# Kernel tuning notes

Hardware: AMD Instinct MI355X
Metric: run time of the kernel (lower is better)

Reference implementation:

```python
import jax, jax.numpy as jnp
import numpy as np

# The 16 differentiable binary logic gates used by difflogic are all of the form
# c0 + c1*a + c2*b + c3*(a*b). Rows are gate ids 0..15.
GATE_COEF = jnp.array([
    [0., 0., 0., 0.],    # 0: False
    [0., 0., 0., 1.],    # 1: a AND b
    [0., 1., 0., -1.],   # 2: a AND NOT b
    [0., 1., 0., 0.],    # 3: a
    [0., 0., 1., -1.],   # 4: NOT a AND b
    [0., 0., 1., 0.],    # 5: b
    [0., 1., 1., -2.],   # 6: XOR
    [0., 1., 1., -1.],   # 7: OR
    [1., -1., -1., 1.],  # 8: NOR
    [1., -1., -1., 2.],  # 9: XNOR
    [1., 0., -1., 0.],   # 10: NOT b
    [1., 0., -1., 1.],   # 11: a OR NOT b (b implies a)
    [1., -1., 0., 0.],   # 12: NOT a
    [1., -1., 0., 1.],   # 13: NOT a OR b (a implies b)
    [1., 0., 0., -1.],   # 14: NAND
    [1., 0., 0., 0.],    # 15: True
], dtype=jnp.float32)

BATCH = 256
IN_DIM = 1024
WIDTH = 64000
K = 10
TAU = 30.0


def _logic_layer(x, w, idx_a, idx_b):
    # x: [B, in_dim], w: [out, 16], idx_*: [out] int32
    a = x[:, idx_a]            # [B, out]
    b = x[:, idx_b]            # [B, out]
    coef = jax.nn.softmax(w, axis=-1) @ GATE_COEF   # [out, 4]
    return coef[:, 0] + coef[:, 1] * a + coef[:, 2] * b + coef[:, 3] * (a * b)


def setup_inputs() -> dict:
    key = jax.random.key(0)
    ks = jax.random.split(key, 10)
    x = jax.random.uniform(ks[0], (BATCH, IN_DIM), dtype=jnp.float32)
    w1 = jax.random.normal(ks[1], (WIDTH, 16), dtype=jnp.float32)
    w2 = jax.random.normal(ks[2], (WIDTH, 16), dtype=jnp.float32)
    w3 = jax.random.normal(ks[3], (WIDTH, 16), dtype=jnp.float32)
    idx_a1 = jax.random.randint(ks[4], (WIDTH,), 0, IN_DIM, dtype=jnp.int32)
    idx_b1 = jax.random.randint(ks[5], (WIDTH,), 0, IN_DIM, dtype=jnp.int32)
    idx_a2 = jax.random.randint(ks[6], (WIDTH,), 0, WIDTH, dtype=jnp.int32)
    idx_b2 = jax.random.randint(ks[7], (WIDTH,), 0, WIDTH, dtype=jnp.int32)
    idx_a3 = jax.random.randint(ks[8], (WIDTH,), 0, WIDTH, dtype=jnp.int32)
    idx_b3 = jax.random.randint(ks[9], (WIDTH,), 0, WIDTH, dtype=jnp.int32)
    return {"x": x, "w1": w1, "w2": w2, "w3": w3,
            "idx_a1": idx_a1, "idx_b1": idx_b1,
            "idx_a2": idx_a2, "idx_b2": idx_b2,
            "idx_a3": idx_a3, "idx_b3": idx_b3}


def reference(x, w1, w2, w3, idx_a1, idx_b1, idx_a2, idx_b2, idx_a3, idx_b3):
    h = _logic_layer(x, w1, idx_a1, idx_b1)
    h = _logic_layer(h, w2, idx_a2, idx_b2)
    h = _logic_layer(h, w3, idx_a3, idx_b3)
    # GroupSum: [B, WIDTH] -> [B, K, WIDTH//K] -> sum -> / tau
    return h.reshape(h.shape[0], K, -1).sum(axis=-1) / TAU
```

## Files before the change

### kernel.cpp

```cpp
#include <hip/hip_runtime.h>
#include <stdint.h>


#define BATCH   256
#define IN_DIM  1024
#define WIDTH   64000
#define NGROUP  10
#define GSIZE   6400
#define TAU     30.0f
#define NWAVE   8
#define GPW     8
#define GPB     (NWAVE*GPW)
#define NBLK    (WIDTH/GPB)

typedef unsigned short ushort_t;

static __device__ __forceinline__ float bf2f(ushort_t s) {
    return __uint_as_float((uint32_t)s << 16);
}
static __device__ __forceinline__ ushort_t f2bf(float f) {
    uint32_t u = __float_as_uint(f);
    return (ushort_t)((u + 0x7fffu + ((u >> 16) & 1u)) >> 16);
}
static __device__ __forceinline__ float gate1(float4 c, float a, float b) {
    return fmaf(b, fmaf(c.w, a, c.z), fmaf(c.y, a, c.x));
}
static __device__ __forceinline__ float4 gate4(float4 c, float4 a, float4 b) {
    float4 r;
    r.x = gate1(c, a.x, b.x);
    r.y = gate1(c, a.y, b.y);
    r.z = gate1(c, a.z, b.z);
    r.w = gate1(c, a.w, b.w);
    return r;
}
static __device__ __forceinline__ float4 up4(ushort4 s) {
    return make_float4(bf2f(s.x), bf2f(s.y), bf2f(s.z), bf2f(s.w));
}

__global__ __launch_bounds__(256) void transpose_kernel(
    const float* __restrict__ x, ushort_t* __restrict__ xT)
{
    __shared__ float tile[64][65];
    const int c0 = (blockIdx.x & 15) * 64;
    const int b0 = (blockIdx.x >> 4) * 64;
    const int lt = threadIdx.x & 63;
    const int wt = threadIdx.x >> 6;
    for (int r = wt; r < 64; r += 4)
        tile[r][lt] = x[(b0 + r) * IN_DIM + c0 + lt];
    __syncthreads();
    for (int r = wt; r < 64; r += 4)
        xT[(c0 + r) * BATCH + b0 + lt] = f2bf(tile[lt][r]);
}

static __device__ __forceinline__ float4 softmax_coef(const float* __restrict__ w)
{
    const float4* w4 = (const float4*)w;
    float4 q0 = w4[0], q1 = w4[1], q2 = w4[2], q3 = w4[3];
    float p[16] = {q0.x,q0.y,q0.z,q0.w, q1.x,q1.y,q1.z,q1.w,
                   q2.x,q2.y,q2.z,q2.w, q3.x,q3.y,q3.z,q3.w};
    float m = p[0];
    #pragma unroll
    for (int i = 1; i < 16; ++i) m = fmaxf(m, p[i]);
    float s = 0.f;
    #pragma unroll
    for (int i = 0; i < 16; ++i) { p[i] = __expf(p[i] - m); s += p[i]; }
    const float inv = 1.0f / s;
    float c0 = (p[8]+p[9]+p[10]+p[11]+p[12]+p[13]+p[14]+p[15]) * inv;
    float c1 = (p[2]+p[3]+p[6]+p[7] - p[8]-p[9]-p[12]-p[13]) * inv;
    float c2 = (p[4]+p[5]+p[6]+p[7] - p[8]-p[9]-p[10]-p[11]) * inv;
    float c3 = (p[1]-p[2]-p[4]-2.f*p[6]-p[7]+p[8]+2.f*p[9]+p[11]+p[13]-p[14]) * inv;
    return make_float4(c0, c1, c2, c3);
}

__global__ __launch_bounds__(256) void prep_kernel(
    const float* __restrict__ w1, const float* __restrict__ w2,
    const float* __restrict__ w3,
    const int* __restrict__ ia1, const int* __restrict__ ib1,
    const int* __restrict__ ia2, const int* __restrict__ ib2,
    const int* __restrict__ ia3, const int* __restrict__ ib3,
    int* __restrict__ leaf,
    float4* __restrict__ pc)
{
    const int j = blockIdx.x * 256 + threadIdx.x;
    if (j >= WIDTH) return;

    const int pa = ia3[j], pb = ib3[j];
    const int qaa = ia2[pa], qab = ib2[pa];
    const int qba = ia2[pb], qbb = ib2[pb];

    int* L = leaf + (size_t)j * 8;
    L[0] = ia1[qaa]; L[1] = ib1[qaa];
    L[2] = ia1[qab]; L[3] = ib1[qab];
    L[4] = ia1[qba]; L[5] = ib1[qba];
    L[6] = ia1[qbb]; L[7] = ib1[qbb];

    float4* P = pc + (size_t)j * 7;
    P[0] = softmax_coef(w1 + (size_t)qaa * 16);
    P[1] = softmax_coef(w1 + (size_t)qab * 16);
    P[2] = softmax_coef(w1 + (size_t)qba * 16);
    P[3] = softmax_coef(w1 + (size_t)qbb * 16);
    P[4] = softmax_coef(w2 + (size_t)pa * 16);
    P[5] = softmax_coef(w2 + (size_t)pb * 16);
    P[6] = softmax_coef(w3 + (size_t)j * 16);
}

__global__ __launch_bounds__(512, 4) void fused_kernel(
    const ushort_t* __restrict__ xT,
    const int*      __restrict__ leaf,
    const float4*   __restrict__ pc,
    float*          __restrict__ red_out)
{
    __shared__ int    sleaf[GPB * 8];
    __shared__ float4 spc[GPB * 7];
    __shared__ float4 sred[NWAVE][64];

    const int tid = threadIdx.x;

    sleaf[tid] = leaf[(size_t)blockIdx.x * (GPB * 8) + tid];
    if (tid < GPB * 7)
        spc[tid] = pc[(size_t)blockIdx.x * (GPB * 7) + tid];
    __syncthreads();

    const int lane = tid & 63;
    const int wave = tid >> 6;
    const int gbase = wave * GPW;

    float4 acc = make_float4(0.f, 0.f, 0.f, 0.f);

    #pragma unroll 2
    for (int u = 0; u < GPW; ++u) {
        const int g = gbase + u;
        const int l0 = __builtin_amdgcn_readfirstlane(sleaf[g*8 + 0]);
        const int l1 = __builtin_amdgcn_readfirstlane(sleaf[g*8 + 1]);
        const int l2 = __builtin_amdgcn_readfirstlane(sleaf[g*8 + 2]);
        const int l3 = __builtin_amdgcn_readfirstlane(sleaf[g*8 + 3]);
        const int l4 = __builtin_amdgcn_readfirstlane(sleaf[g*8 + 4]);
        const int l5 = __builtin_amdgcn_readfirstlane(sleaf[g*8 + 5]);
        const int l6 = __builtin_amdgcn_readfirstlane(sleaf[g*8 + 6]);
        const int l7 = __builtin_amdgcn_readfirstlane(sleaf[g*8 + 7]);

        const ushort4 v0 = ((const ushort4*)(xT + (size_t)l0 * BATCH))[lane];
        const ushort4 v1 = ((const ushort4*)(xT + (size_t)l1 * BATCH))[lane];
        const ushort4 v2 = ((const ushort4*)(xT + (size_t)l2 * BATCH))[lane];
        const ushort4 v3 = ((const ushort4*)(xT + (size_t)l3 * BATCH))[lane];
        const ushort4 v4 = ((const ushort4*)(xT + (size_t)l4 * BATCH))[lane];
        const ushort4 v5 = ((const ushort4*)(xT + (size_t)l5 * BATCH))[lane];
        const ushort4 v6 = ((const ushort4*)(xT + (size_t)l6 * BATCH))[lane];
        const ushort4 v7 = ((const ushort4*)(xT + (size_t)l7 * BATCH))[lane];

        const float4 C1aa = spc[g*7 + 0];
        const float4 C1ab = spc[g*7 + 1];
        const float4 C1ba = spc[g*7 + 2];
        const float4 C1bb = spc[g*7 + 3];
        const float4 C2a  = spc[g*7 + 4];
        const float4 C2b  = spc[g*7 + 5];
        const float4 C3c  = spc[g*7 + 6];

        const float4 haa = gate4(C1aa, up4(v0), up4(v1));
        const float4 hab = gate4(C1ab, up4(v2), up4(v3));
        const float4 hba = gate4(C1ba, up4(v4), up4(v5));
        const float4 hbb = gate4(C1bb, up4(v6), up4(v7));
        const float4 h2a = gate4(C2a, haa, hab);
        const float4 h2b = gate4(C2b, hba, hbb);
        const float4 h3  = gate4(C3c, h2a, h2b);
        acc.x += h3.x; acc.y += h3.y; acc.z += h3.z; acc.w += h3.w;
    }

    sred[wave][lane] = acc;
    __syncthreads();
    if (wave == 0) {
        float4 t = sred[0][lane];
        #pragma unroll
        for (int w = 1; w < NWAVE; ++w) {
            float4 q = sred[w][lane];
            t.x += q.x; t.y += q.y; t.z += q.z; t.w += q.w;
        }
        const float sc = 1.0f / TAU;
        const int grp = (blockIdx.x * GPB) / GSIZE;
        const int b0 = lane * 4;
        atomicAdd(&red_out[(b0 + 0) * NGROUP + grp], t.x * sc);
        atomicAdd(&red_out[(b0 + 1) * NGROUP + grp], t.y * sc);
        atomicAdd(&red_out[(b0 + 2) * NGROUP + grp], t.z * sc);
        atomicAdd(&red_out[(b0 + 3) * NGROUP + grp], t.w * sc);
    }
}

extern "C" void kernel_launch(void* const* d_in, const int* in_sizes, int n_in,
                              void* d_out, int out_size, void* d_ws, size_t ws_size,
                              hipStream_t stream)
{
    const float* x   = (const float*)d_in[0];
    const float* w1  = (const float*)d_in[1];
    const float* w2  = (const float*)d_in[2];
    const float* w3  = (const float*)d_in[3];
    const int*   ia1 = (const int*)d_in[4];
    const int*   ib1 = (const int*)d_in[5];
    const int*   ia2 = (const int*)d_in[6];
    const int*   ib2 = (const int*)d_in[7];
    const int*   ia3 = (const int*)d_in[8];
    const int*   ib3 = (const int*)d_in[9];
    float* out = (float*)d_out;

    char* ws = (char*)d_ws;
    ushort_t* xT = (ushort_t*)ws;
    int*    leaf = (int*)(ws + (size_t)IN_DIM * BATCH * 2);
    float4*   pc = (float4*)(leaf + (size_t)WIDTH * 8);

    hipMemsetAsync(d_out, 0, (size_t)out_size * sizeof(float), stream);

    transpose_kernel<<<64, 256, 0, stream>>>(x, xT);
    prep_kernel<<<WIDTH / 256, 256, 0, stream>>>(w1, w2, w3,
                                                 ia1, ib1, ia2, ib2, ia3, ib3,
                                                 leaf, pc);
    fused_kernel<<<NBLK, 512, 0, stream>>>(xT, leaf, pc, out);
}
```

Baseline: 150.3 us.

## Precompute per-gate softmax coefficients once and software-pipeline leaf gathers

Adds a coef_kernel that computes the softmax-derived gate coefficients once per gate in each layer, so prep_kernel gathers them instead of recomputing seven softmaxes per output, which repeated layer-1 and layer-2 work. The fused kernel now double-buffers the leaf gathers across two register sets so the loads for the next group are in flight while the current group is computed. It also unpacks bf16 values from uint2 words with shift and mask, and lowers launch_bounds minimum occupancy from 4 to 2 to leave room for the extra registers. This costs one more kernel launch and extra workspace.

```diff
diff --git a/kernel.cpp b/kernel.cpp
--- a/kernel.cpp
+++ b/kernel.cpp
@@ -15,12 +15,15 @@
 
 typedef unsigned short ushort_t;
 
-static __device__ __forceinline__ float bf2f(ushort_t s) {
-    return __uint_as_float((uint32_t)s << 16);
-}
 static __device__ __forceinline__ ushort_t f2bf(float f) {
     uint32_t u = __float_as_uint(f);
     return (ushort_t)((u + 0x7fffu + ((u >> 16) & 1u)) >> 16);
+}
+static __device__ __forceinline__ float bfl(uint32_t u) {
+    return __uint_as_float(u << 16);
+}
+static __device__ __forceinline__ float bfh(uint32_t u) {
+    return __uint_as_float(u & 0xffff0000u);
 }
 static __device__ __forceinline__ float gate1(float4 c, float a, float b) {
     return fmaf(b, fmaf(c.w, a, c.z), fmaf(c.y, a, c.x));
@@ -33,8 +36,13 @@
     r.w = gate1(c, a.w, b.w);
     return r;
 }
-static __device__ __forceinline__ float4 up4(ushort4 s) {
-    return make_float4(bf2f(s.x), bf2f(s.y), bf2f(s.z), bf2f(s.w));
+static __device__ __forceinline__ float4 gate4p(float4 c, uint2 a, uint2 b) {
+    float4 r;
+    r.x = gate1(c, bfl(a.x), bfl(b.x));
+    r.y = gate1(c, bfh(a.x), bfh(b.x));
+    r.z = gate1(c, bfl(a.y), bfl(b.y));
+    r.w = gate1(c, bfh(a.y), bfh(b.y));
+    return r;
 }
 
 __global__ __launch_bounds__(256) void transpose_kernel(
@@ -52,9 +60,18 @@
         xT[(c0 + r) * BATCH + b0 + lt] = f2bf(tile[lt][r]);
 }
 
-static __device__ __forceinline__ float4 softmax_coef(const float* __restrict__ w)
-{
-    const float4* w4 = (const float4*)w;
+__global__ __launch_bounds__(256) void coef_kernel(
+    const float* __restrict__ w1, const float* __restrict__ w2,
+    const float* __restrict__ w3,
+    float4* __restrict__ c1o, float4* __restrict__ c2o, float4* __restrict__ c3o)
+{
+    const int id = blockIdx.x * 256 + threadIdx.x;
+    const int layer = id / WIDTH;
+    const int j = id - layer * WIDTH;
+    const float* w = (layer == 0) ? w1 : (layer == 1) ? w2 : w3;
+    float4* cc     = (layer == 0) ? c1o : (layer == 1) ? c2o : c3o;
+
+    const float4* w4 = (const float4*)(w + (size_t)j * 16);
     float4 q0 = w4[0], q1 = w4[1], q2 = w4[2], q3 = w4[3];
     float p[16] = {q0.x,q0.y,q0.z,q0.w, q1.x,q1.y,q1.z,q1.w,
                    q2.x,q2.y,q2.z,q2.w, q3.x,q3.y,q3.z,q3.w};
@@ -69,15 +86,15 @@
     float c1 = (p[2]+p[3]+p[6]+p[7] - p[8]-p[9]-p[12]-p[13]) * inv;
     float c2 = (p[4]+p[5]+p[6]+p[7] - p[8]-p[9]-p[10]-p[11]) * inv;
     float c3 = (p[1]-p[2]-p[4]-2.f*p[6]-p[7]+p[8]+2.f*p[9]+p[11]+p[13]-p[14]) * inv;
-    return make_float4(c0, c1, c2, c3);
+    cc[j] = make_float4(c0, c1, c2, c3);
 }
 
 __global__ __launch_bounds__(256) void prep_kernel(
-    const float* __restrict__ w1, const float* __restrict__ w2,
-    const float* __restrict__ w3,
     const int* __restrict__ ia1, const int* __restrict__ ib1,
     const int* __restrict__ ia2, const int* __restrict__ ib2,
     const int* __restrict__ ia3, const int* __restrict__ ib3,
+    const float4* __restrict__ c1, const float4* __restrict__ c2,
+    const float4* __restrict__ c3,
     int* __restrict__ leaf,
     float4* __restrict__ pc)
 {
@@ -95,16 +112,44 @@
     L[6] = ia1[qbb]; L[7] = ib1[qbb];
 
     float4* P = pc + (size_t)j * 7;
-    P[0] = softmax_coef(w1 + (size_t)qaa * 16);
-    P[1] = softmax_coef(w1 + (size_t)qab * 16);
-    P[2] = softmax_coef(w1 + (size_t)qba * 16);
-    P[3] = softmax_coef(w1 + (size_t)qbb * 16);
-    P[4] = softmax_coef(w2 + (size_t)pa * 16);
-    P[5] = softmax_coef(w2 + (size_t)pb * 16);
-    P[6] = softmax_coef(w3 + (size_t)j * 16);
-}
-
-__global__ __launch_bounds__(512, 4) void fused_kernel(
+    P[0] = c1[qaa]; P[1] = c1[qab]; P[2] = c1[qba]; P[3] = c1[qbb];
+    P[4] = c2[pa];  P[5] = c2[pb];
+    P[6] = c3[j];
+}
+
+#define LOADG(q0,q1,q2,q3,q4,q5,q6,q7, g) do {                                 \
+    const int _g8 = (g) * 8;                                                   \
+    const int _c0 = __builtin_amdgcn_readfirstlane(sleaf[_g8 + 0]);            \
+    const int _c1 = __builtin_amdgcn_readfirstlane(sleaf[_g8 + 1]);            \
+    const int _c2 = __builtin_amdgcn_readfirstlane(sleaf[_g8 + 2]);            \
+    const int _c3 = __builtin_amdgcn_readfirstlane(sleaf[_g8 + 3]);            \
+    const int _c4 = __builtin_amdgcn_readfirstlane(sleaf[_g8 + 4]);            \
+    const int _c5 = __builtin_amdgcn_readfirstlane(sleaf[_g8 + 5]);            \
+    const int _c6 = __builtin_amdgcn_readfirstlane(sleaf[_g8 + 6]);            \
+    const int _c7 = __builtin_amdgcn_readfirstlane(sleaf[_g8 + 7]);            \
+    q0 = ((const uint2*)(xT + (size_t)_c0 * BATCH))[lane];                     \
+    q1 = ((const uint2*)(xT + (size_t)_c1 * BATCH))[lane];                     \
+    q2 = ((const uint2*)(xT + (size_t)_c2 * BATCH))[lane];                     \
+    q3 = ((const uint2*)(xT + (size_t)_c3 * BATCH))[lane];                     \
+    q4 = ((const uint2*)(xT + (size_t)_c4 * BATCH))[lane];                     \
+    q5 = ((const uint2*)(xT + (size_t)_c5 * BATCH))[lane];                     \
+    q6 = ((const uint2*)(xT + (size_t)_c6 * BATCH))[lane];                     \
+    q7 = ((const uint2*)(xT + (size_t)_c7 * BATCH))[lane];                     \
+} while (0)
+
+#define COMPG(q0,q1,q2,q3,q4,q5,q6,q7, g) do {                                 \
+    const int _g7 = (g) * 7;                                                   \
+    const float4 _haa = gate4p(spc[_g7 + 0], q0, q1);                          \
+    const float4 _hab = gate4p(spc[_g7 + 1], q2, q3);                          \
+    const float4 _hba = gate4p(spc[_g7 + 2], q4, q5);                          \
+    const float4 _hbb = gate4p(spc[_g7 + 3], q6, q7);                          \
+    const float4 _h2a = gate4(spc[_g7 + 4], _haa, _hab);                       \
+    const float4 _h2b = gate4(spc[_g7 + 5], _hba, _hbb);                       \
+    const float4 _h3  = gate4(spc[_g7 + 6], _h2a, _h2b);                       \
+    acc.x += _h3.x; acc.y += _h3.y; acc.z += _h3.z; acc.w += _h3.w;            \
+} while (0)
+
+__global__ __launch_bounds__(512, 2) void fused_kernel(
     const ushort_t* __restrict__ xT,
     const int*      __restrict__ leaf,
     const float4*   __restrict__ pc,
@@ -123,48 +168,30 @@
 
     const int lane = tid & 63;
     const int wave = tid >> 6;
-    const int gbase = wave * GPW;
+    const int g0 = wave * GPW;
+
+    uint2 A0, A1, A2, A3, A4, A5, A6, A7;
+    uint2 B0, B1, B2, B3, B4, B5, B6, B7;
+
+    LOADG(A0,A1,A2,A3,A4,A5,A6,A7, g0 + 0);
+    LOADG(B0,B1,B2,B3,B4,B5,B6,B7, g0 + 1);
 
     float4 acc = make_float4(0.f, 0.f, 0.f, 0.f);
 
-    #pragma unroll 2
-    for (int u = 0; u < GPW; ++u) {
-        const int g = gbase + u;
-        const int l0 = __builtin_amdgcn_readfirstlane(sleaf[g*8 + 0]);
-        const int l1 = __builtin_amdgcn_readfirstlane(sleaf[g*8 + 1]);
-        const int l2 = __builtin_amdgcn_readfirstlane(sleaf[g*8 + 2]);
-        const int l3 = __builtin_amdgcn_readfirstlane(sleaf[g*8 + 3]);
-        const int l4 = __builtin_amdgcn_readfirstlane(sleaf[g*8 + 4]);
-        const int l5 = __builtin_amdgcn_readfirstlane(sleaf[g*8 + 5]);
-        const int l6 = __builtin_amdgcn_readfirstlane(sleaf[g*8 + 6]);
-        const int l7 = __builtin_amdgcn_readfirstlane(sleaf[g*8 + 7]);
-
-        const ushort4 v0 = ((const ushort4*)(xT + (size_t)l0 * BATCH))[lane];
-        const ushort4 v1 = ((const ushort4*)(xT + (size_t)l1 * BATCH))[lane];
-        const ushort4 v2 = ((const ushort4*)(xT + (size_t)l2 * BATCH))[lane];
-        const ushort4 v3 = ((const ushort4*)(xT + (size_t)l3 * BATCH))[lane];
-        const ushort4 v4 = ((const ushort4*)(xT + (size_t)l4 * BATCH))[lane];
-        const ushort4 v5 = ((const ushort4*)(xT + (size_t)l5 * BATCH))[lane];
-        const ushort4 v6 = ((const ushort4*)(xT + (size_t)l6 * BATCH))[lane];
-        const ushort4 v7 = ((const ushort4*)(xT + (size_t)l7 * BATCH))[lane];
-
-        const float4 C1aa = spc[g*7 + 0];
-        const float4 C1ab = spc[g*7 + 1];
-        const float4 C1ba = spc[g*7 + 2];
-        const float4 C1bb = spc[g*7 + 3];
-        const float4 C2a  = spc[g*7 + 4];
-        const float4 C2b  = spc[g*7 + 5];
-        const float4 C3c  = spc[g*7 + 6];
-
-        const float4 haa = gate4(C1aa, up4(v0), up4(v1));
-        const float4 hab = gate4(C1ab, up4(v2), up4(v3));
-        const float4 hba = gate4(C1ba, up4(v4), up4(v5));
-        const float4 hbb = gate4(C1bb, up4(v6), up4(v7));
-        const float4 h2a = gate4(C2a, haa, hab);
-        const float4 h2b = gate4(C2b, hba, hbb);
-        const float4 h3  = gate4(C3c, h2a, h2b);
-        acc.x += h3.x; acc.y += h3.y; acc.z += h3.z; acc.w += h3.w;
-    }
+    COMPG(A0,A1,A2,A3,A4,A5,A6,A7, g0 + 0);
+    LOADG(A0,A1,A2,A3,A4,A5,A6,A7, g0 + 2);
+    COMPG(B0,B1,B2,B3,B4,B5,B6,B7, g0 + 1);
+    LOADG(B0,B1,B2,B3,B4,B5,B6,B7, g0 + 3);
+    COMPG(A0,A1,A2,A3,A4,A5,A6,A7, g0 + 2);
+    LOADG(A0,A1,A2,A3,A4,A5,A6,A7, g0 + 4);
+    COMPG(B0,B1,B2,B3,B4,B5,B6,B7, g0 + 3);
+    LOADG(B0,B1,B2,B3,B4,B5,B6,B7, g0 + 5);
+    COMPG(A0,A1,A2,A3,A4,A5,A6,A7, g0 + 4);
+    LOADG(A0,A1,A2,A3,A4,A5,A6,A7, g0 + 6);
+    COMPG(B0,B1,B2,B3,B4,B5,B6,B7, g0 + 5);
+    LOADG(B0,B1,B2,B3,B4,B5,B6,B7, g0 + 7);
+    COMPG(A0,A1,A2,A3,A4,A5,A6,A7, g0 + 6);
+    COMPG(B0,B1,B2,B3,B4,B5,B6,B7, g0 + 7);
 
     sred[wave][lane] = acc;
     __syncthreads();
@@ -205,12 +232,15 @@
     ushort_t* xT = (ushort_t*)ws;
     int*    leaf = (int*)(ws + (size_t)IN_DIM * BATCH * 2);
     float4*   pc = (float4*)(leaf + (size_t)WIDTH * 8);
+    float4*   c1 = pc + (size_t)WIDTH * 7;
+    float4*   c2 = c1 + WIDTH;
+    float4*   c3 = c2 + WIDTH;
 
     hipMemsetAsync(d_out, 0, (size_t)out_size * sizeof(float), stream);
 
     transpose_kernel<<<64, 256, 0, stream>>>(x, xT);
-    prep_kernel<<<WIDTH / 256, 256, 0, stream>>>(w1, w2, w3,
-                                                 ia1, ib1, ia2, ib2, ia3, ib3,
-                                                 leaf, pc);
+    coef_kernel<<<(3 * WIDTH) / 256, 256, 0, stream>>>(w1, w2, w3, c1, c2, c3);
+    prep_kernel<<<WIDTH / 256, 256, 0, stream>>>(ia1, ib1, ia2, ib2, ia3, ib3,
+                                                 c1, c2, c3, leaf, pc);
     fused_kernel<<<NBLK, 512, 0, stream>>>(xT, leaf, pc, out);
 }
```

After: 221.0 us. +47.1%, slower.
